# Optimization experiments

Hardware: AMD Instinct MI355X
Metric: run time of the kernel (lower is better)

The kernel has to match this reference:

```python
import jax, jax.numpy as jnp
import numpy as np

B, T, C = 4, 2048, 1024
H = 16
DH = C // H
DFF = 4 * C


def _layernorm(x, g, b, eps=1e-5):
    mu = jnp.mean(x, axis=-1, keepdims=True)
    var = jnp.var(x, axis=-1, keepdims=True)
    return (x - mu) * jax.lax.rsqrt(var + eps) * g + b


def setup_inputs() -> dict:
    key = jax.random.key(0)
    ks = jax.random.split(key, 12)
    s = 0.02
    return {
        "x": jax.random.normal(ks[0], (B, T, C), jnp.float32),
        "Wq": jax.random.normal(ks[1], (H, C, DH), jnp.float32) * s,
        "bq": jnp.zeros((H, DH), jnp.float32),
        "Wk": jax.random.normal(ks[2], (H, C, DH), jnp.float32) * s,
        "bk": jnp.zeros((H, DH), jnp.float32),
        "Wv": jax.random.normal(ks[3], (H, C, DH), jnp.float32) * s,
        "bv": jnp.zeros((H, DH), jnp.float32),
        "Wo": jax.random.normal(ks[4], (C, C), jnp.float32) * s,
        "bo": jnp.zeros((C,), jnp.float32),
        "ln1_g": jnp.ones((C,), jnp.float32),
        "ln1_b": jnp.zeros((C,), jnp.float32),
        "ln2_g": jnp.ones((C,), jnp.float32),
        "ln2_b": jnp.zeros((C,), jnp.float32),
        "W1": jax.random.normal(ks[5], (C, DFF), jnp.float32) * s,
        "b1": jnp.zeros((DFF,), jnp.float32),
        "W2": jax.random.normal(ks[6], (DFF, C), jnp.float32) * s,
        "b2": jnp.zeros((C,), jnp.float32),
    }


def reference(x, Wq, bq, Wk, bk, Wv, bv, Wo, bo, ln1_g, ln1_b, ln2_g, ln2_b, W1, b1, W2, b2):
    # pre-norm for attention
    xn = _layernorm(x, ln1_g, ln1_b)
    # per-head projections, batched: [B,H,T,DH]
    q = jnp.einsum("btc,hcd->bhtd", xn, Wq) + bq[None, :, None, :]
    k = jnp.einsum("btc,hcd->bhtd", xn, Wk) + bk[None, :, None, :]
    v = jnp.einsum("btc,hcd->bhtd", xn, Wv) + bv[None, :, None, :]
    # FAITHFUL to source: scores / scale with scale = DH**-0.5, i.e. * sqrt(DH)
    scores = jnp.einsum("bhtd,bhsd->bhts", q, k) * jnp.sqrt(jnp.float32(DH))
    attn = jax.nn.softmax(scores, axis=-1)
    o = jnp.einsum("bhts,bhsd->bhtd", attn, v)  # [B,H,T,DH]
    # concat heads along last dim (head order matches ModuleList concat)
    o = jnp.transpose(o, (0, 2, 1, 3)).reshape(B, T, C)
    attn_out = o @ Wo + bo  # dropout is identity at eval
    x = x + attn_out
    xn2 = _layernorm(x, ln2_g, ln2_b)
    ffn = jax.nn.relu(xn2 @ W1 + b1) @ W2 + b2
    return x + ffn
```

## Files before the change

### kernel.cpp

```cpp
#include <hip/hip_runtime.h>
#include <hip/hip_bf16.h>
#include <stdint.h>

typedef unsigned short ushort_t;
typedef short short8 __attribute__((ext_vector_type(8)));
typedef unsigned short ushortx8 __attribute__((ext_vector_type(8)));
typedef float floatx4 __attribute__((ext_vector_type(4)));

__device__ __forceinline__ float b2f(ushort_t u) {
    return __uint_as_float(((unsigned int)u) << 16);
}
__device__ __forceinline__ ushort_t f2bf(float f) {
    unsigned int u = __float_as_uint(f);
    unsigned int r = u + 0x7FFFu + ((u >> 16) & 1u);
    return (ushort_t)(r >> 16);
}
__device__ __forceinline__ void gll16(const void* g, void* l) {
    __builtin_amdgcn_global_load_lds((const __attribute__((address_space(1))) unsigned int*)g,
                                     (__attribute__((address_space(3))) unsigned int*)l,
                                     16, 0, 0);
}

__global__ void transpose_kernel(const float* __restrict__ in, ushort_t* __restrict__ out,
                                 int K, int N) {
    __shared__ float tile[32][33];
    in += (long)blockIdx.z * K * N;
    out += (long)blockIdx.z * K * N;
    int k0 = blockIdx.x * 32, n0 = blockIdx.y * 32;
    int x = threadIdx.x, y = threadIdx.y;
#pragma unroll
    for (int i = 0; i < 4; i++)
        tile[y + 8 * i][x] = in[(long)(k0 + y + 8 * i) * N + n0 + x];
    __syncthreads();
#pragma unroll
    for (int i = 0; i < 4; i++)
        out[(long)(n0 + y + 8 * i) * K + k0 + x] = f2bf(tile[x][y + 8 * i]);
}

__global__ void concat_bias_kernel(const float* __restrict__ bq, const float* __restrict__ bk,
                                   const float* __restrict__ bv, float* __restrict__ dst) {
    int i = blockIdx.x * 256 + threadIdx.x;
    dst[i] = i < 1024 ? bq[i] : (i < 2048 ? bk[i - 1024] : bv[i - 2048]);
}

__global__ __launch_bounds__(256) void ln_kernel(const float* __restrict__ in,
                                                 ushort_t* __restrict__ out,
                                                 const float* __restrict__ g,
                                                 const float* __restrict__ b) {
    long row = blockIdx.x;
    int tid = threadIdx.x;
    float4 v4 = *((const float4*)(in + row * 1024) + tid);
    float v[4] = {v4.x, v4.y, v4.z, v4.w};
    float s1 = v[0] + v[1] + v[2] + v[3];
    float s2 = v[0] * v[0] + v[1] * v[1] + v[2] * v[2] + v[3] * v[3];
#pragma unroll
    for (int m = 32; m >= 1; m >>= 1) {
        s1 += __shfl_xor(s1, m);
        s2 += __shfl_xor(s2, m);
    }
    __shared__ float r1[4], r2[4];
    int w = tid >> 6;
    if ((tid & 63) == 0) { r1[w] = s1; r2[w] = s2; }
    __syncthreads();
    s1 = r1[0] + r1[1] + r1[2] + r1[3];
    s2 = r2[0] + r2[1] + r2[2] + r2[3];
    float mu = s1 * (1.0f / 1024.0f);
    float var = s2 * (1.0f / 1024.0f) - mu * mu;
    float inv = rsqrtf(var + 1e-5f);
    float y[4];
#pragma unroll
    for (int i = 0; i < 4; i++)
        y[i] = (v[i] - mu) * inv * g[tid * 4 + i] + b[tid * 4 + i];
    unsigned int lo = (unsigned int)f2bf(y[0]) | ((unsigned int)f2bf(y[1]) << 16);
    unsigned int hi = (unsigned int)f2bf(y[2]) | ((unsigned int)f2bf(y[3]) << 16);
    *(uint2*)(out + row * 1024 + tid * 4) = make_uint2(lo, hi);
}

template <typename OutT, int RELU, int MODE>
__device__ __forceinline__ void gemm128(
    const ushort_t* __restrict__ A, int lda,
    const ushort_t* __restrict__ Bt, int ldb, int K,
    OutT* __restrict__ C, long cBatch, int ldc,
    const float* __restrict__ bias, const float* __restrict__ resid,
    ushort_t* As, ushort_t* Bs) {
    int m0 = blockIdx.x * 128, n0 = blockIdx.y * 128;
    int tid = threadIdx.x, lane = tid & 63, w = tid >> 6;
    int ln = lane & 15, quad = lane >> 4;
    int wr = w >> 1, wc = w & 1;
    int lr = lane >> 2, lc = (lane & 3) * 8;

    auto stage = [&](int k0, int buf) {
#pragma unroll
        for (int i = 0; i < 4; i++) {
            int id = w * 4 + i;
            int blk = id & 7;
            int row = blk * 16 + lr;
            if (id < 8)
                gll16(A + (long)(m0 + row) * lda + k0 + lc, As + buf * 4096 + blk * 512);
            else
                gll16(Bt + (long)(n0 + row) * ldb + k0 + lc, Bs + buf * 4096 + blk * 512);
        }
    };

    floatx4 acc[4][4];
#pragma unroll
    for (int a = 0; a < 4; a++)
#pragma unroll
        for (int bb = 0; bb < 4; bb++) acc[a][bb] = floatx4{0, 0, 0, 0};

    stage(0, 0);
    int cur = 0;
    for (int k0 = 0; k0 < K; k0 += 32, cur ^= 1) {
        __syncthreads();
        if (k0 + 32 < K) stage(k0 + 32, cur ^ 1);
        const ushort_t* Ab = As + cur * 4096;
        const ushort_t* Bb = Bs + cur * 4096;
        short8 af[4], bf[4];
#pragma unroll
        for (int j = 0; j < 4; j++) {
            af[j] = *(const short8*)(Ab + (wr * 64 + j * 16 + ln) * 32 + quad * 8);
            bf[j] = *(const short8*)(Bb + (wc * 64 + j * 16 + ln) * 32 + quad * 8);
        }
#pragma unroll
        for (int a = 0; a < 4; a++)
#pragma unroll
            for (int bb = 0; bb < 4; bb++)
                acc[a][bb] = __builtin_amdgcn_mfma_f32_16x16x32_bf16(af[a], bf[bb], acc[a][bb], 0, 0, 0);
    }
#pragma unroll
    for (int bb = 0; bb < 4; bb++) {
        int gn = n0 + wc * 64 + bb * 16 + ln;
        float bv = bias ? bias[gn] : 0.0f;
#pragma unroll
        for (int a = 0; a < 4; a++) {
#pragma unroll
            for (int r = 0; r < 4; r++) {
                int gm = m0 + wr * 64 + a * 16 + quad * 4 + r;
                float val = acc[a][bb][r] + bv;
                if (RELU) val = fmaxf(val, 0.0f);
                if constexpr (MODE == 2) {
                    int gnl = gn & 1023;
                    long off;
                    if (gn < 2048)
                        off = (long)(gn >> 10) * 8388608 + (long)(gm >> 11) * 2097152 +
                              (long)(gm & 2047) * 1024 + gnl;
                    else
                        off = 16777216L +
                              ((((long)(gm >> 11)) * 16 + (gnl >> 6)) * 64 + (gnl & 63)) * 2048 +
                              (gm & 2047);
                    C[off] = (OutT)f2bf(val);
                } else {
                    long off = (long)(gm >> 11) * cBatch + (long)(gm & 2047) * ldc + gn;
                    if (resid) val += resid[off];
                    if constexpr (sizeof(OutT) == 2)
                        C[off] = (OutT)f2bf(val);
                    else
                        C[off] = (OutT)val;
                }
            }
        }
    }
}

__global__ __launch_bounds__(256) void gemm128_qkv_kernel(
    const ushort_t* __restrict__ A, const ushort_t* __restrict__ Bt,
    ushort_t* __restrict__ C, const float* __restrict__ bias) {
    __shared__ ushort_t As[2 * 128 * 32];
    __shared__ ushort_t Bs[2 * 128 * 32];
    gemm128<ushort_t, 0, 2>(A, 1024, Bt, 1024, 1024, C, 0, 0, bias, nullptr, As, Bs);
}

__global__ __launch_bounds__(256) void gemm128_bf16_relu_kernel(
    const ushort_t* __restrict__ A, int lda, const ushort_t* __restrict__ Bt, int ldb, int K,
    ushort_t* __restrict__ C, long cBatch, int ldc, const float* __restrict__ bias) {
    __shared__ ushort_t As[2 * 128 * 32];
    __shared__ ushort_t Bs[2 * 128 * 32];
    gemm128<ushort_t, 1, 0>(A, lda, Bt, ldb, K, C, cBatch, ldc, bias, nullptr, As, Bs);
}

__global__ __launch_bounds__(256) void gemm128_f32_kernel(
    const ushort_t* __restrict__ A, int lda, const ushort_t* __restrict__ Bt, int ldb, int K,
    float* __restrict__ C, long cBatch, int ldc,
    const float* __restrict__ bias, const float* __restrict__ resid) {
    __shared__ ushort_t As[2 * 128 * 32];
    __shared__ ushort_t Bs[2 * 128 * 32];
    gemm128<float, 0, 0>(A, lda, Bt, ldb, K, C, cBatch, ldc, bias, resid, As, Bs);
}

__global__ __launch_bounds__(256, 3) void attn_kernel(
    const ushort_t* __restrict__ q, const ushort_t* __restrict__ k,
    const ushort_t* __restrict__ vt, ushort_t* __restrict__ o) {
    __shared__ ushort_t Klds[2 * 4096];
    __shared__ ushort_t Vlds[2 * 4096];
    __shared__ ushort_t Plds[4 * 32 * 68];
    int flat = blockIdx.x;
    int bh = (flat & 7) * 8 + (flat >> 7);
    int xt = (flat >> 3) & 15;
    int b = bh >> 4, h = bh & 15;
    int t0 = xt * 128;
    int tid = threadIdx.x, lane = tid & 63, w = tid >> 6;
    int ln = lane & 15, quad = lane >> 4;
    int lr = lane >> 2, lc = (lane & 3) * 8;

    const ushort_t* qbase = q + ((long)b * 2048 + t0 + w * 32) * 1024 + h * 64;
    short8 qf[2][2];
#pragma unroll
    for (int sub = 0; sub < 2; sub++)
#pragma unroll
        for (int s = 0; s < 2; s++) {
            ushortx8 t = *(const ushortx8*)(qbase + (long)(sub * 16 + ln) * 1024 + s * 32 + quad * 8);
#pragma unroll
            for (int j = 0; j < 8; j++) qf[sub][s][j] = (short)f2bf(b2f(t[j]) * 8.0f);
        }

    floatx4 O[2][4];
    float m_i[2][4], l_i[2][4];
#pragma unroll
    for (int sub = 0; sub < 2; sub++)
#pragma unroll
        for (int i = 0; i < 4; i++) {
            O[sub][i] = floatx4{0, 0, 0, 0};
            m_i[sub][i] = -1e30f;
            l_i[sub][i] = 0.0f;
        }

    short8 ones;
#pragma unroll
    for (int j = 0; j < 8; j++) ones[j] = (short)0x3F80;

    ushort_t* Pw = Plds + w * 32 * 68;
    long krow0 = (long)b * 2048 * 1024 + h * 64;
    const ushort_t* vbase = vt + (long)bh * 64 * 2048;

    auto stage = [&](int kv0, int buf) {
#pragma unroll
        for (int i = 0; i < 4; i++) {
            int id = w * 4 + i;
            int hh = (id >> 2) & 1, qt = id & 3;
            int row = qt * 16 + lr;
            if (id < 8)
                gll16(k + krow0 + (long)(kv0 + row) * 1024 + hh * 32 + lc,
                      Klds + buf * 4096 + hh * 2048 + qt * 512);
            else
                gll16(vbase + (long)row * 2048 + kv0 + hh * 32 + lc,
                      Vlds + buf * 4096 + hh * 2048 + qt * 512);
        }
    };

    stage(0, 0);
    int cur = 0;
    for (int t32 = 0; t32 < 32; t32++, cur ^= 1) {
        __syncthreads();
        if (t32 < 31) stage((t32 + 1) * 64, cur ^ 1);
        const ushort_t* Kb = Klds + cur * 4096;
        const ushort_t* Vb = Vlds + cur * 4096;

        floatx4 S[2][4];
#pragma unroll
        for (int sub = 0; sub < 2; sub++)
#pragma unroll
            for (int nc = 0; nc < 4; nc++) S[sub][nc] = floatx4{0, 0, 0, 0};
#pragma unroll
        for (int s = 0; s < 2; s++)
#pragma unroll
            for (int nc = 0; nc < 4; nc++) {
                short8 kf = *(const short8*)(Kb + s * 2048 + (nc * 16 + ln) * 32 + quad * 8);
                S[0][nc] = __builtin_amdgcn_mfma_f32_16x16x32_bf16(qf[0][s], kf, S[0][nc], 0, 0, 0);
                S[1][nc] = __builtin_amdgcn_mfma_f32_16x16x32_bf16(qf[1][s], kf, S[1][nc], 0, 0, 0);
            }
        float alpha[2][4];
#pragma unroll
        for (int sub = 0; sub < 2; sub++) {
#pragma unroll
            for (int r = 0; r < 4; r++) {
                float mx = fmaxf(fmaxf(S[sub][0][r], S[sub][1][r]),
                                 fmaxf(S[sub][2][r], S[sub][3][r]));
#pragma unroll
                for (int msk = 1; msk <= 8; msk <<= 1) mx = fmaxf(mx, __shfl_xor(mx, msk));
                float nm = fmaxf(m_i[sub][r], mx);
                alpha[sub][r] = __expf(m_i[sub][r] - nm);
                m_i[sub][r] = nm;
            }
#pragma unroll
            for (int nc = 0; nc < 4; nc++)
#pragma unroll
                for (int r = 0; r < 4; r++) {
                    float p = __expf(S[sub][nc][r] - m_i[sub][r]);
                    Pw[(sub * 16 + quad * 4 + r) * 68 + nc * 16 + ln] = f2bf(p);
                }
        }
        short8 pf[2][2];
#pragma unroll
        for (int sub = 0; sub < 2; sub++)
#pragma unroll
            for (int s = 0; s < 2; s++)
                pf[sub][s] = *(const short8*)(Pw + (sub * 16 + ln) * 68 + s * 32 + quad * 8);
#pragma unroll
        for (int sub = 0; sub < 2; sub++) {
            floatx4 L = floatx4{0, 0, 0, 0};
            L = __builtin_amdgcn_mfma_f32_16x16x32_bf16(pf[sub][0], ones, L, 0, 0, 0);
            L = __builtin_amdgcn_mfma_f32_16x16x32_bf16(pf[sub][1], ones, L, 0, 0, 0);
#pragma unroll
            for (int r = 0; r < 4; r++) l_i[sub][r] = l_i[sub][r] * alpha[sub][r] + L[r];
#pragma unroll
            for (int dc = 0; dc < 4; dc++)
#pragma unroll
                for (int r = 0; r < 4; r++) O[sub][dc][r] *= alpha[sub][r];
        }
#pragma unroll
        for (int s = 0; s < 2; s++)
#pragma unroll
            for (int dc = 0; dc < 4; dc++) {
                short8 vf = *(const short8*)(Vb + s * 2048 + (dc * 16 + ln) * 32 + quad * 8);
                O[0][dc] = __builtin_amdgcn_mfma_f32_16x16x32_bf16(pf[0][s], vf, O[0][dc], 0, 0, 0);
                O[1][dc] = __builtin_amdgcn_mfma_f32_16x16x32_bf16(pf[1][s], vf, O[1][dc], 0, 0, 0);
            }
    }
#pragma unroll
    for (int sub = 0; sub < 2; sub++)
#pragma unroll
        for (int r = 0; r < 4; r++) {
            float inv = 1.0f / l_i[sub][r];
            int t = t0 + w * 32 + sub * 16 + quad * 4 + r;
            ushort_t* orow = o + ((long)b * 2048 + t) * 1024 + h * 64;
#pragma unroll
            for (int dc = 0; dc < 4; dc++) orow[dc * 16 + ln] = f2bf(O[sub][dc][r] * inv);
        }
}

extern "C" void kernel_launch(void* const* d_in, const int* in_sizes, int n_in,
                              void* d_out, int out_size, void* d_ws, size_t ws_size,
                              hipStream_t stream) {
    const float* x   = (const float*)d_in[0];
    const float* Wq  = (const float*)d_in[1];
    const float* bq  = (const float*)d_in[2];
    const float* Wk  = (const float*)d_in[3];
    const float* bk  = (const float*)d_in[4];
    const float* Wv  = (const float*)d_in[5];
    const float* bv  = (const float*)d_in[6];
    const float* Wo  = (const float*)d_in[7];
    const float* bo  = (const float*)d_in[8];
    const float* g1  = (const float*)d_in[9];
    const float* be1 = (const float*)d_in[10];
    const float* g2  = (const float*)d_in[11];
    const float* be2 = (const float*)d_in[12];
    const float* W1  = (const float*)d_in[13];
    const float* b1  = (const float*)d_in[14];
    const float* W2  = (const float*)d_in[15];
    const float* b2  = (const float*)d_in[16];
    float* out = (float*)d_out;

    const long MB = 1 << 20;
    char* w = (char*)d_ws;
    ushort_t* xn  = (ushort_t*)(w);
    float*    x2  = (float*)(w + 16 * MB);
    ushort_t* qb  = (ushort_t*)(w + 48 * MB);
    ushort_t* kb  = (ushort_t*)(w + 64 * MB);
    ushort_t* vtb = (ushort_t*)(w + 80 * MB);
    ushort_t* xn2 = qb;
    ushort_t* h1  = (ushort_t*)(w + 64 * MB);
    ushort_t* WqT = (ushort_t*)(w + 96 * MB);
    ushort_t* WkT = (ushort_t*)(w + 98 * MB);
    ushort_t* WvT = (ushort_t*)(w + 100 * MB);
    ushort_t* WoT = (ushort_t*)(w + 102 * MB);
    ushort_t* W1T = (ushort_t*)(w + 104 * MB);
    ushort_t* W2T = (ushort_t*)(w + 112 * MB);
    float* biasCat = x2;

    dim3 tb(32, 8);
    transpose_kernel<<<dim3(32, 2, 16), tb, 0, stream>>>(Wq, WqT, 1024, 64);
    transpose_kernel<<<dim3(32, 2, 16), tb, 0, stream>>>(Wk, WkT, 1024, 64);
    transpose_kernel<<<dim3(32, 2, 16), tb, 0, stream>>>(Wv, WvT, 1024, 64);
    transpose_kernel<<<dim3(32, 32, 1), tb, 0, stream>>>(Wo, WoT, 1024, 1024);
    transpose_kernel<<<dim3(32, 128, 1), tb, 0, stream>>>(W1, W1T, 1024, 4096);
    transpose_kernel<<<dim3(128, 32, 1), tb, 0, stream>>>(W2, W2T, 4096, 1024);
    concat_bias_kernel<<<12, 256, 0, stream>>>(bq, bk, bv, biasCat);

    ln_kernel<<<8192, 256, 0, stream>>>(x, xn, g1, be1);
    gemm128_qkv_kernel<<<dim3(64, 24), 256, 0, stream>>>(xn, WqT, qb, biasCat);
    attn_kernel<<<1024, 256, 0, stream>>>(qb, kb, vtb, xn );
    gemm128_f32_kernel<<<dim3(64, 8), 256, 0, stream>>>(xn, 1024, WoT, 1024, 1024,
                                                        x2, 2048L * 1024, 1024, bo, x);
    ln_kernel<<<8192, 256, 0, stream>>>((const float*)x2, xn2, g2, be2);
    gemm128_bf16_relu_kernel<<<dim3(64, 16), 256, 0, stream>>>(
        xn2, 1024, W1T, 1024, 1024, h1, 2048L * 2048, 2048, b1);
    gemm128_f32_kernel<<<dim3(64, 8), 256, 0, stream>>>(
        h1, 2048, W2T, 4096, 2048, out, 2048L * 1024, 1024, b2, x2);
    gemm128_bf16_relu_kernel<<<dim3(64, 16), 256, 0, stream>>>(
        xn2, 1024, W1T + 2048L * 1024, 1024, 1024, h1, 2048L * 2048, 2048, b1 + 2048);
    gemm128_f32_kernel<<<dim3(64, 8), 256, 0, stream>>>(
        h1, 2048, W2T + 2048, 4096, 2048, out, 2048L * 1024, 1024, nullptr, out);
}
```

Measured before the change: 702.6 us.

## Enlarge attention blocks to 8 waves and compute transposed scores for cheaper softmax

Attention blocks grow to 512 threads covering 256 query rows, so each staged K/V tile in LDS is reused by twice as many waves. Scores are now computed as K·Q^T, which puts one query row per lane column. The row max and row sum then need only two cross-lane shuffles, and the ones-vector MFMA used for row sums goes away. P values are written to LDS as packed pairs, and the rescale factors are redistributed with shuffles. In exchange, occupancy and register pressure change under the new launch bounds, and the per-row statistics must be shuffled back into the layout of the O accumulator.

Measured after the change: 640.0 us. -8.9%, faster.

```diff
diff --git a/kernel.cpp b/kernel.cpp
--- a/kernel.cpp
+++ b/kernel.cpp
@@ -14,6 +14,9 @@
     unsigned int u = __float_as_uint(f);
     unsigned int r = u + 0x7FFFu + ((u >> 16) & 1u);
     return (ushort_t)(r >> 16);
+}
+__device__ __forceinline__ unsigned int pack2bf(float a, float b) {
+    return (unsigned int)f2bf(a) | ((unsigned int)f2bf(b) << 16);
 }
 __device__ __forceinline__ void gll16(const void* g, void* l) {
     __builtin_amdgcn_global_load_lds((const __attribute__((address_space(1))) unsigned int*)g,
@@ -187,20 +190,22 @@
     gemm128<float, 0, 0>(A, lda, Bt, ldb, K, C, cBatch, ldc, bias, resid, As, Bs);
 }
 
-__global__ __launch_bounds__(256, 3) void attn_kernel(
+#define PSTR 72
+__global__ __launch_bounds__(512, 4) void attn_kernel(
     const ushort_t* __restrict__ q, const ushort_t* __restrict__ k,
     const ushort_t* __restrict__ vt, ushort_t* __restrict__ o) {
     __shared__ ushort_t Klds[2 * 4096];
     __shared__ ushort_t Vlds[2 * 4096];
-    __shared__ ushort_t Plds[4 * 32 * 68];
+    __shared__ ushort_t Plds[8 * 32 * PSTR];
     int flat = blockIdx.x;
-    int bh = (flat & 7) * 8 + (flat >> 7);
-    int xt = (flat >> 3) & 15;
+    int bh = (flat & 7) * 8 + (flat >> 6);
+    int xt = (flat >> 3) & 7;
     int b = bh >> 4, h = bh & 15;
-    int t0 = xt * 128;
+    int t0 = xt * 256;
     int tid = threadIdx.x, lane = tid & 63, w = tid >> 6;
     int ln = lane & 15, quad = lane >> 4;
     int lr = lane >> 2, lc = (lane & 3) * 8;
+    int bsrc = (lane & 48) + ((lane >> 4) << 2);
 
     const ushort_t* qbase = q + ((long)b * 2048 + t0 + w * 32) * 1024 + h * 64;
     short8 qf[2][2];
@@ -214,36 +219,28 @@
         }
 
     floatx4 O[2][4];
-    float m_i[2][4], l_i[2][4];
+    float m_i[2] = {-1e30f, -1e30f}, l_i[2] = {0.0f, 0.0f};
 #pragma unroll
     for (int sub = 0; sub < 2; sub++)
 #pragma unroll
-        for (int i = 0; i < 4; i++) {
-            O[sub][i] = floatx4{0, 0, 0, 0};
-            m_i[sub][i] = -1e30f;
-            l_i[sub][i] = 0.0f;
-        }
-
-    short8 ones;
-#pragma unroll
-    for (int j = 0; j < 8; j++) ones[j] = (short)0x3F80;
-
-    ushort_t* Pw = Plds + w * 32 * 68;
+        for (int i = 0; i < 4; i++) O[sub][i] = floatx4{0, 0, 0, 0};
+
+    ushort_t* Pw = Plds + w * 32 * PSTR;
     long krow0 = (long)b * 2048 * 1024 + h * 64;
     const ushort_t* vbase = vt + (long)bh * 64 * 2048;
 
     auto stage = [&](int kv0, int buf) {
 #pragma unroll
-        for (int i = 0; i < 4; i++) {
-            int id = w * 4 + i;
-            int hh = (id >> 2) & 1, qt = id & 3;
+        for (int i = 0; i < 2; i++) {
+            int id = w * 2 + i;
+            int s = (id >> 2) & 1, qt = id & 3;
             int row = qt * 16 + lr;
             if (id < 8)
-                gll16(k + krow0 + (long)(kv0 + row) * 1024 + hh * 32 + lc,
-                      Klds + buf * 4096 + hh * 2048 + qt * 512);
+                gll16(k + krow0 + (long)(kv0 + row) * 1024 + s * 32 + lc,
+                      Klds + buf * 4096 + s * 2048 + qt * 512);
             else
-                gll16(vbase + (long)row * 2048 + kv0 + hh * 32 + lc,
-                      Vlds + buf * 4096 + hh * 2048 + qt * 512);
+                gll16(vbase + (long)row * 2048 + kv0 + s * 32 + lc,
+                      Vlds + buf * 4096 + s * 2048 + qt * 512);
         }
     };
 
@@ -255,72 +252,68 @@
         const ushort_t* Kb = Klds + cur * 4096;
         const ushort_t* Vb = Vlds + cur * 4096;
 
-        floatx4 S[2][4];
-#pragma unroll
-        for (int sub = 0; sub < 2; sub++)
-#pragma unroll
-            for (int nc = 0; nc < 4; nc++) S[sub][nc] = floatx4{0, 0, 0, 0};
-#pragma unroll
-        for (int s = 0; s < 2; s++)
+        float alpha[2];
+#pragma unroll
+        for (int sub = 0; sub < 2; sub++) {
+            floatx4 Z[4];
+#pragma unroll
+            for (int nc = 0; nc < 4; nc++) Z[nc] = floatx4{0, 0, 0, 0};
+#pragma unroll
+            for (int s = 0; s < 2; s++)
+#pragma unroll
+                for (int nc = 0; nc < 4; nc++) {
+                    short8 kf = *(const short8*)(Kb + s * 2048 + (nc * 16 + ln) * 32 + quad * 8);
+                    Z[nc] = __builtin_amdgcn_mfma_f32_16x16x32_bf16(kf, qf[sub][s], Z[nc], 0, 0, 0);
+                }
+            float mx = -1e30f;
+#pragma unroll
+            for (int nc = 0; nc < 4; nc++)
+#pragma unroll
+                for (int r = 0; r < 4; r++) mx = fmaxf(mx, Z[nc][r]);
+            mx = fmaxf(mx, __shfl_xor(mx, 16));
+            mx = fmaxf(mx, __shfl_xor(mx, 32));
+            float nm = fmaxf(m_i[sub], mx);
+            alpha[sub] = __expf(m_i[sub] - nm);
+            m_i[sub] = nm;
+            float rs = 0.0f;
+            ushort_t* Ps = Pw + sub * 16 * PSTR + ln * PSTR;
 #pragma unroll
             for (int nc = 0; nc < 4; nc++) {
-                short8 kf = *(const short8*)(Kb + s * 2048 + (nc * 16 + ln) * 32 + quad * 8);
-                S[0][nc] = __builtin_amdgcn_mfma_f32_16x16x32_bf16(qf[0][s], kf, S[0][nc], 0, 0, 0);
-                S[1][nc] = __builtin_amdgcn_mfma_f32_16x16x32_bf16(qf[1][s], kf, S[1][nc], 0, 0, 0);
+                float p0 = __expf(Z[nc][0] - nm), p1 = __expf(Z[nc][1] - nm);
+                float p2 = __expf(Z[nc][2] - nm), p3 = __expf(Z[nc][3] - nm);
+                rs += (p0 + p1) + (p2 + p3);
+                *(uint2*)(Ps + nc * 16 + quad * 4) = make_uint2(pack2bf(p0, p1), pack2bf(p2, p3));
             }
-        float alpha[2][4];
+            rs += __shfl_xor(rs, 16);
+            rs += __shfl_xor(rs, 32);
+            l_i[sub] = l_i[sub] * alpha[sub] + rs;
+        }
 #pragma unroll
         for (int sub = 0; sub < 2; sub++) {
 #pragma unroll
             for (int r = 0; r < 4; r++) {
-                float mx = fmaxf(fmaxf(S[sub][0][r], S[sub][1][r]),
-                                 fmaxf(S[sub][2][r], S[sub][3][r]));
-#pragma unroll
-                for (int msk = 1; msk <= 8; msk <<= 1) mx = fmaxf(mx, __shfl_xor(mx, msk));
-                float nm = fmaxf(m_i[sub][r], mx);
-                alpha[sub][r] = __expf(m_i[sub][r] - nm);
-                m_i[sub][r] = nm;
+                float ar = __shfl(alpha[sub], bsrc + r);
+#pragma unroll
+                for (int dc = 0; dc < 4; dc++) O[sub][dc][r] *= ar;
             }
-#pragma unroll
-            for (int nc = 0; nc < 4; nc++)
-#pragma unroll
-                for (int r = 0; r < 4; r++) {
-                    float p = __expf(S[sub][nc][r] - m_i[sub][r]);
-                    Pw[(sub * 16 + quad * 4 + r) * 68 + nc * 16 + ln] = f2bf(p);
+            short8 pf[2];
+#pragma unroll
+            for (int s = 0; s < 2; s++)
+                pf[s] = *(const short8*)(Pw + (sub * 16 + ln) * PSTR + s * 32 + quad * 8);
+#pragma unroll
+            for (int s = 0; s < 2; s++)
+#pragma unroll
+                for (int dc = 0; dc < 4; dc++) {
+                    short8 vf = *(const short8*)(Vb + s * 2048 + (dc * 16 + ln) * 32 + quad * 8);
+                    O[sub][dc] = __builtin_amdgcn_mfma_f32_16x16x32_bf16(pf[s], vf, O[sub][dc], 0, 0, 0);
                 }
         }
-        short8 pf[2][2];
-#pragma unroll
-        for (int sub = 0; sub < 2; sub++)
-#pragma unroll
-            for (int s = 0; s < 2; s++)
-                pf[sub][s] = *(const short8*)(Pw + (sub * 16 + ln) * 68 + s * 32 + quad * 8);
-#pragma unroll
-        for (int sub = 0; sub < 2; sub++) {
-            floatx4 L = floatx4{0, 0, 0, 0};
-            L = __builtin_amdgcn_mfma_f32_16x16x32_bf16(pf[sub][0], ones, L, 0, 0, 0);
-            L = __builtin_amdgcn_mfma_f32_16x16x32_bf16(pf[sub][1], ones, L, 0, 0, 0);
-#pragma unroll
-            for (int r = 0; r < 4; r++) l_i[sub][r] = l_i[sub][r] * alpha[sub][r] + L[r];
-#pragma unroll
-            for (int dc = 0; dc < 4; dc++)
-#pragma unroll
-                for (int r = 0; r < 4; r++) O[sub][dc][r] *= alpha[sub][r];
-        }
-#pragma unroll
-        for (int s = 0; s < 2; s++)
-#pragma unroll
-            for (int dc = 0; dc < 4; dc++) {
-                short8 vf = *(const short8*)(Vb + s * 2048 + (dc * 16 + ln) * 32 + quad * 8);
-                O[0][dc] = __builtin_amdgcn_mfma_f32_16x16x32_bf16(pf[0][s], vf, O[0][dc], 0, 0, 0);
-                O[1][dc] = __builtin_amdgcn_mfma_f32_16x16x32_bf16(pf[1][s], vf, O[1][dc], 0, 0, 0);
-            }
     }
 #pragma unroll
     for (int sub = 0; sub < 2; sub++)
 #pragma unroll
         for (int r = 0; r < 4; r++) {
-            float inv = 1.0f / l_i[sub][r];
+            float inv = 1.0f / __shfl(l_i[sub], bsrc + r);
             int t = t0 + w * 32 + sub * 16 + quad * 4 + r;
             ushort_t* orow = o + ((long)b * 2048 + t) * 1024 + h * 64;
 #pragma unroll
@@ -378,7 +371,7 @@
 
     ln_kernel<<<8192, 256, 0, stream>>>(x, xn, g1, be1);
     gemm128_qkv_kernel<<<dim3(64, 24), 256, 0, stream>>>(xn, WqT, qb, biasCat);
-    attn_kernel<<<1024, 256, 0, stream>>>(qb, kb, vtb, xn );
+    attn_kernel<<<512, 512, 0, stream>>>(qb, kb, vtb, xn );
     gemm128_f32_kernel<<<dim3(64, 8), 256, 0, stream>>>(xn, 1024, WoT, 1024, 1024,
                                                         x2, 2048L * 1024, 1024, bo, x);
     ln_kernel<<<8192, 256, 0, stream>>>((const float*)x2, xn2, g2, be2);
```
